# Kernel tuning notes

Hardware: AMD Instinct MI355X
Metric: run time of the kernel (lower is better)

## Reference

```python
import jax, jax.numpy as jnp
import numpy as np

EMBED_DIM = 1024
NUM_HEADS = 16
HEAD_DIM = EMBED_DIM // NUM_HEADS
EPS = 1e-6


def setup_inputs() -> dict:
    key = jax.random.key(0)
    ks = jax.random.split(key, 11)
    Lq, Lk, N = 4096, 4096, 4
    s = 1.0 / np.sqrt(EMBED_DIM)
    inp = {
        'q': jax.random.normal(ks[0], (Lq, N, EMBED_DIM), dtype=jnp.float32),
        'k': jax.random.normal(ks[1], (Lk, N, EMBED_DIM), dtype=jnp.float32),
        'v': jax.random.normal(ks[2], (Lk, N, EMBED_DIM), dtype=jnp.float32),
        'Wq': jax.random.normal(ks[3], (EMBED_DIM, EMBED_DIM), dtype=jnp.float32) * s,
        'bq': jax.random.normal(ks[4], (EMBED_DIM,), dtype=jnp.float32) * s,
        'Wk': jax.random.normal(ks[5], (EMBED_DIM, EMBED_DIM), dtype=jnp.float32) * s,
        'bk': jax.random.normal(ks[6], (EMBED_DIM,), dtype=jnp.float32) * s,
        'Wv': jax.random.normal(ks[7], (EMBED_DIM, EMBED_DIM), dtype=jnp.float32) * s,
        'bv': jax.random.normal(ks[8], (EMBED_DIM,), dtype=jnp.float32) * s,
        'Wo': jax.random.normal(ks[9], (EMBED_DIM, EMBED_DIM), dtype=jnp.float32) * s,
        'bo': jax.random.normal(ks[10], (EMBED_DIM,), dtype=jnp.float32) * s,
    }
    return inp


def _feature_map(x):
    # F.elu(x) + 1
    return jax.nn.elu(x) + 1.0


def reference(q, k, v, Wq, bq, Wk, bk, Wv, bv, Wo, bo):
    Lq, N, E = q.shape
    Lk = k.shape[0]
    # torch Linear: y = x @ W.T + b
    qp = q @ Wq.T + bq
    kp = k @ Wk.T + bk
    vp = v @ Wv.T + bv
    # (L, N, E) -> (N, H, L, D)
    qh = qp.reshape(Lq, N, NUM_HEADS, HEAD_DIM).transpose(1, 2, 0, 3)
    kh = kp.reshape(Lk, N, NUM_HEADS, HEAD_DIM).transpose(1, 2, 0, 3)
    vh = vp.reshape(Lk, N, NUM_HEADS, HEAD_DIM).transpose(1, 2, 0, 3)
    qf = _feature_map(qh)
    kf = _feature_map(kh)
    k_sum = kf.sum(axis=2)                               # (N, H, D)
    kv = jnp.einsum('nhld,nhle->nhde', kf, vh)            # (N, H, D, D)
    z = 1.0 / (jnp.einsum('nhld,nhd->nhl', qf, k_sum) + EPS)
    out = jnp.einsum('nhld,nhde->nhle', qf, kv) * z[..., None]
    out = out.transpose(2, 0, 1, 3).reshape(Lq, N, E)
    out = out @ Wo.T + bo
    return out
```

## Files before the change

kernel.cpp:

```cpp
#include <hip/hip_runtime.h>
#include <hip/hip_bf16.h>
#include <cstdint>


typedef __attribute__((ext_vector_type(8))) short bf16x8;
typedef __attribute__((ext_vector_type(4))) float f32x4;

#define L_SEQ 4096
#define NBATCH 4
#define EMB 1024
#define NHEADS 16
#define HDIM 64
#define MROWS (L_SEQ * NBATCH)
#define NHG (NBATCH * NHEADS)
#define LCHUNK 512
#define NCHUNK (L_SEQ / LCHUNK)

__device__ __forceinline__ unsigned short f2bf(float f) {
  union { float f; uint32_t u; } v; v.f = f;
  uint32_t u = v.u;
  u += 0x7fffu + ((u >> 16) & 1u);
  return (unsigned short)(u >> 16);
}
__device__ __forceinline__ float bf2f(unsigned short s) {
  union { uint32_t u; float f; } v; v.u = ((uint32_t)s) << 16;
  return v.f;
}
__device__ __forceinline__ uint32_t pkbf(float a, float b) {
  union { float f; uint32_t u; } ua, ub; ua.f = a; ub.f = b;
  return ((ua.u + 0x8000u) >> 16) | ((ub.u + 0x8000u) & 0xffff0000u);
}

__global__ __launch_bounds__(256) void convert_kernel(const float* __restrict__ src,
                                                      unsigned short* __restrict__ dst,
                                                      int n) {
  int i = (blockIdx.x * 256 + threadIdx.x) * 4;
  if (i + 4 <= n) {
    float4 f = *(const float4*)(src + i);
    uint2 p;
    p.x = pkbf(f.x, f.y);
    p.y = pkbf(f.z, f.w);
    *(uint2*)(dst + i) = p;
  }
}

__global__ __launch_bounds__(256) void convert_w4(const float* __restrict__ s0,
                                                  const float* __restrict__ s1,
                                                  const float* __restrict__ s2,
                                                  const float* __restrict__ s3,
                                                  unsigned short* __restrict__ d0,
                                                  unsigned short* __restrict__ d1,
                                                  unsigned short* __restrict__ d2,
                                                  unsigned short* __restrict__ d3,
                                                  int n) {
  const int w = blockIdx.y;
  const float* src = (w == 0) ? s0 : (w == 1) ? s1 : (w == 2) ? s2 : s3;
  unsigned short* dst = (w == 0) ? d0 : (w == 1) ? d1 : (w == 2) ? d2 : d3;
  int i = (blockIdx.x * 256 + threadIdx.x) * 4;
  if (i + 4 <= n) {
    float4 f = *(const float4*)(src + i);
    uint2 p;
    p.x = pkbf(f.x, f.y);
    p.y = pkbf(f.z, f.w);
    *(uint2*)(dst + i) = p;
  }
}


#define STAGE_H(MATB, RH, SLOT, KTN)                                            \
  do {                                                                          \
    _Pragma("unroll")                                                           \
    for (int r_ = 0; r_ < 2; r_++) {                                            \
      const long grow_ = ((MATB) ? bcol0 : arow0) + (RH) * 128 + r_ * 64 + srowt;\
      const unsigned short* gp_ =                                               \
          ((MATB) ? B : A) + grow_ * (long)K + (KTN) + skoff;                   \
      __builtin_amdgcn_global_load_lds(                                         \
          (const __attribute__((address_space(1))) void*)gp_,                   \
          (__attribute__((address_space(3))) void*)(smem + (MATB) * 65536 +     \
              (SLOT) * 16384 + r_ * 8192 + wid * 1024),                         \
          16, 0, 0);                                                            \
    }                                                                           \
  } while (0)

#define MFMA_Q(AF, BF, MFB, NFB)                                                \
  do {                                                                          \
    __builtin_amdgcn_s_setprio(1);                                              \
    _Pragma("unroll")                                                           \
    for (int mi_ = 0; mi_ < 4; mi_++)                                           \
      _Pragma("unroll")                                                         \
      for (int ni_ = 0; ni_ < 2; ni_++)                                         \
        _Pragma("unroll")                                                       \
        for (int ks_ = 0; ks_ < 2; ks_++)                                       \
          acc[(MFB) + mi_][(NFB) + ni_] =                                       \
              __builtin_amdgcn_mfma_f32_16x16x32_bf16(                          \
                  AF[mi_ * 2 + ks_], BF[ni_ * 2 + ks_],                         \
                  acc[(MFB) + mi_][(NFB) + ni_], 0, 0, 0);                      \
    __builtin_amdgcn_s_setprio(0);                                              \
  } while (0)

#define PH_SYNC                                                                 \
  __builtin_amdgcn_s_barrier();                                                 \
  asm volatile("s_waitcnt lgkmcnt(0)" ::: "memory");                            \
  __builtin_amdgcn_sched_barrier(0);

#define TILE_T(SA, K1, K2, S01, S23, VMODE)                                     \
  do {                                                                          \
    bf16x8 af0[8], af1[8], bf0[4], bf1[4];                                      \
             \
    _Pragma("unroll")                                                           \
    for (int mi_ = 0; mi_ < 4; mi_++)                                           \
      _Pragma("unroll")                                                         \
      for (int ks_ = 0; ks_ < 2; ks_++)                                         \
        af0[mi_ * 2 + ks_] = *(const bf16x8*)(smem + ((SA) + wr) * 16384 + aRB +\
                                              mi_ * 2048 + akt[ks_]);           \
    _Pragma("unroll")                                                           \
    for (int ni_ = 0; ni_ < 2; ni_++)                                           \
      _Pragma("unroll")                                                         \
      for (int ks_ = 0; ks_ < 2; ks_++)                                         \
        bf0[ni_ * 2 + ks_] = *(const bf16x8*)(smem + 65536 +                    \
                                              ((SA) + (wc >> 1)) * 16384 + bRB +\
                                              ni_ * 2048 + akt[ks_]);           \
    if (S01) STAGE_H(0, 1, (SA) ^ 3, K1);                                       \
    PH_SYNC                                                                     \
    MFMA_Q(af0, bf0, 0, 0);                                                     \
    __builtin_amdgcn_s_barrier();                                               \
                                      \
    _Pragma("unroll")                                                           \
    for (int ni_ = 0; ni_ < 2; ni_++)                                           \
      _Pragma("unroll")                                                         \
      for (int ks_ = 0; ks_ < 2; ks_++)                                         \
        bf1[ni_ * 2 + ks_] = *(const bf16x8*)(smem + 65536 +                    \
                                              ((SA) + (wc >> 1)) * 16384 + bRB +\
                                              (ni_ + 2) * 2048 + akt[ks_]);     \
    if (S01) STAGE_H(1, 1, (SA) ^ 3, K1);                                       \
    PH_SYNC                                                                     \
    MFMA_Q(af0, bf1, 0, 2);                                                     \
    __builtin_amdgcn_s_barrier();                                               \
                                  \
    _Pragma("unroll")                                                           \
    for (int mi_ = 0; mi_ < 4; mi_++)                                           \
      _Pragma("unroll")                                                         \
      for (int ks_ = 0; ks_ < 2; ks_++)                                         \
        af1[mi_ * 2 + ks_] = *(const bf16x8*)(smem + ((SA) + wr) * 16384 + aRB +\
                                              (mi_ + 4) * 2048 + akt[ks_]);     \
    if (S23) STAGE_H(1, 0, (SA), K2);                                           \
    PH_SYNC                                                                     \
    MFMA_Q(af1, bf1, 4, 2);                                                     \
    __builtin_amdgcn_s_barrier();                                               \
                     \
    if (S23) STAGE_H(0, 0, (SA), K2);                                           \
    PH_SYNC                                                                     \
    MFMA_Q(af1, bf0, 4, 0);                                                     \
    if ((VMODE) == 1) asm volatile("s_waitcnt vmcnt(4)" ::: "memory");          \
    if ((VMODE) == 2) asm volatile("s_waitcnt vmcnt(0)" ::: "memory");          \
    __builtin_amdgcn_s_barrier();                                               \
  } while (0)

template <int MODE>
__global__ __launch_bounds__(512, 2) void gemm_bt(const unsigned short* __restrict__ A,
                                                  const unsigned short* __restrict__ B,
                                                  const float* __restrict__ bias,
                                                  void* __restrict__ Cout,
                                                  int M, int Nn, int K) {
  __shared__ __align__(16) char smem[131072];

  const int tid   = threadIdx.x;
  const int wid   = tid >> 6;
  const int lane  = tid & 63;
  const int col16 = lane & 15;
  const int quad  = lane >> 4;
  const int wr = wid >> 2;
  const int wc = wid & 3;
  const long arow0 = (long)blockIdx.x * 256;
  const long bcol0 = (long)blockIdx.y * 256;

  const int axor = (col16 & 7) << 4;
  int akt[2];
  akt[0] = (quad * 16) ^ axor;
  akt[1] = (64 + quad * 16) ^ axor;
  const int aRB = col16 * 128;
  const int bRB = ((wc & 1) * 64 + col16) * 128;

  const int srowt = tid >> 3;
  const int skoff = (((tid & 7) * 16) ^ ((srowt & 7) << 4)) >> 1;

  const int NT = K >> 6;

  STAGE_H(0, 0, 0, 0);
  STAGE_H(0, 1, 1, 0);
  STAGE_H(1, 0, 0, 0);
  STAGE_H(1, 1, 1, 0);
  STAGE_H(1, 0, 2, 64);
  STAGE_H(0, 0, 2, 64);

  const f32x4 fzero = {0.f, 0.f, 0.f, 0.f};
  f32x4 acc[8][4];
#pragma unroll
  for (int i = 0; i < 8; i++)
#pragma unroll
    for (int j = 0; j < 4; j++) acc[i][j] = fzero;

  asm volatile("s_waitcnt vmcnt(4)" ::: "memory");
  __builtin_amdgcn_s_barrier();

#pragma unroll 1
  for (int u = 0; u + 4 <= NT; u += 2) {
    TILE_T(0, (u + 1) * 64, (u + 2) * 64, 1, 1, 1);
    TILE_T(2, (u + 2) * 64, (u + 3) * 64, 1, 1, 1);
  }
  TILE_T(0, (NT - 1) * 64, 0, 1, 0, 2);
  TILE_T(2, 0, 0, 0, 0, 0);

  float bcol[4];
#pragma unroll
  for (int nf = 0; nf < 4; nf++) bcol[nf] = bias[bcol0 + wc * 64 + nf * 16 + col16];

  const int erow = tid >> 4;
  const int ecc  = tid & 15;

  if (MODE != 2) {
    unsigned short* epi = (unsigned short*)smem;
    const int EST = 264;
#pragma unroll
    for (int s = 0; s < 8; s++) {
      if ((s >> 2) == wr) {
        const int mfb = (s & 3) * 2;
#pragma unroll
        for (int ml = 0; ml < 2; ml++)
#pragma unroll
          for (int nf = 0; nf < 4; nf++)
#pragma unroll
            for (int rr = 0; rr < 4; rr++) {
              float vv = acc[mfb + ml][nf][rr] + bcol[nf];
              if (MODE == 0) vv = (vv > 0.f) ? (vv + 1.f) : __expf(vv);
              epi[(ml * 16 + quad * 4 + rr) * EST + wc * 64 + nf * 16 + col16] =
                  f2bf(vv);
            }
      }
      __syncthreads();
      {
        const long gr = arow0 + s * 32 + erow;
        const unsigned short* srcp = &epi[erow * EST + ecc * 16];
        uint4 a  = *(const uint4*)srcp;
        uint4 b2 = *(const uint4*)(srcp + 8);
        unsigned short* Cp = (unsigned short*)Cout + gr * Nn + bcol0 + ecc * 16;
        *(uint4*)Cp       = a;
        *(uint4*)(Cp + 8) = b2;
      }
      __syncthreads();
    }
  } else {
    float* epi = (float*)smem;
    const int ESF = 260;
#pragma unroll
    for (int s = 0; s < 8; s++) {
      if ((s >> 2) == wr) {
        const int mfb = (s & 3) * 2;
#pragma unroll
        for (int ml = 0; ml < 2; ml++)
#pragma unroll
          for (int nf = 0; nf < 4; nf++)
#pragma unroll
            for (int rr = 0; rr < 4; rr++)
              epi[(ml * 16 + quad * 4 + rr) * ESF + wc * 64 + nf * 16 + col16] =
                  acc[mfb + ml][nf][rr] + bcol[nf];
      }
      __syncthreads();
      {
        const long gr = arow0 + s * 32 + erow;
        const float* srcp = &epi[erow * ESF + ecc * 16];
        float* Cp = (float*)Cout + gr * Nn + bcol0 + ecc * 16;
#pragma unroll
        for (int s4 = 0; s4 < 4; s4++)
          *(float4*)(Cp + s4 * 4) = *(const float4*)(srcp + s4 * 4);
      }
      __syncthreads();
    }
  }
}

__global__ __launch_bounds__(256) void kv_partial_kernel(const unsigned short* __restrict__ kf,
                                                         const unsigned short* __restrict__ vp,
                                                         float* __restrict__ kvp,
                                                         float* __restrict__ ksp) {
  __shared__ float ks[32 * 64];
  __shared__ float vs[32 * 64];
  const int hg = blockIdx.x;
  const int chunk = blockIdx.y;
  const int n = hg >> 4, h = hg & 15;
  const int tid = threadIdx.x;
  const int td = tid >> 4, te = tid & 15;
  const long hoff = (long)n * EMB + h * HDIM;
  const int l0 = chunk * LCHUNK;

  float acc[4][4];
#pragma unroll
  for (int i = 0; i < 4; i++)
#pragma unroll
    for (int j = 0; j < 4; j++) acc[i][j] = 0.f;
  float ksacc[4] = {0.f, 0.f, 0.f, 0.f};

  const int lrow = tid >> 3;
  const int dcol = (tid & 7) * 8;

  for (int ls = 0; ls < LCHUNK; ls += 32) {
    const long g = (long)(l0 + ls + lrow) * (NBATCH * EMB) + hoff + dcol;
    uint4 kr = *(const uint4*)(kf + g);
    uint4 vr = *(const uint4*)(vp + g);
    float* kd = &ks[lrow * 64 + dcol];
    float* vd = &vs[lrow * 64 + dcol];
    uint32_t ku[4] = {kr.x, kr.y, kr.z, kr.w};
    uint32_t vu[4] = {vr.x, vr.y, vr.z, vr.w};
#pragma unroll
    for (int t2 = 0; t2 < 4; t2++) {
      kd[2 * t2]     = bf2f((unsigned short)(ku[t2] & 0xffffu));
      kd[2 * t2 + 1] = bf2f((unsigned short)(ku[t2] >> 16));
      vd[2 * t2]     = bf2f((unsigned short)(vu[t2] & 0xffffu));
      vd[2 * t2 + 1] = bf2f((unsigned short)(vu[t2] >> 16));
    }
    __syncthreads();
#pragma unroll
    for (int l = 0; l < 32; l++) {
      float kq[4], vq[4];
      *(float4*)kq = *(const float4*)(&ks[l * 64 + td * 4]);
      *(float4*)vq = *(const float4*)(&vs[l * 64 + te * 4]);
#pragma unroll
      for (int i = 0; i < 4; i++) {
        ksacc[i] += kq[i];
#pragma unroll
        for (int j = 0; j < 4; j++) acc[i][j] += kq[i] * vq[j];
      }
    }
    __syncthreads();
  }
  float* outp = kvp + ((long)chunk * NHG + hg) * 4096;
#pragma unroll
  for (int i = 0; i < 4; i++)
#pragma unroll
    for (int j = 0; j < 4; j++)
      outp[(td * 4 + i) * 64 + te * 4 + j] = acc[i][j];
  if (te == 0) {
    float* o2 = ksp + ((long)chunk * NHG + hg) * 64;
#pragma unroll
    for (int i = 0; i < 4; i++) o2[td * 4 + i] = ksacc[i];
  }
}

__global__ __launch_bounds__(256) void attn_out_kernel(const unsigned short* __restrict__ qf,
                                                       const float* __restrict__ kvp,
                                                       const float* __restrict__ ksp,
                                                       unsigned short* __restrict__ out1) {
  __shared__ __align__(16) char smem[53248];
  const int hg = blockIdx.x;
  const int lc = blockIdx.y;
  const int n = hg >> 4, h = hg & 15;
  const int tid = threadIdx.x;
  const int wid = tid >> 6;
  const int lane = tid & 63;
  const int col16 = lane & 15;
  const int quad  = lane >> 4;
  const long lbase = (long)lc * 256;

#pragma unroll
  for (int r = 0; r < 8; r++) {
    const int row = r * 32 + (tid >> 3);
    const long l = lbase + row;
    const int sk = (((tid & 7) * 16) ^ ((row & 7) << 4)) >> 1;
    const unsigned short* gp = qf + (l * NBATCH + n) * (long)EMB + h * HDIM + sk;
    __builtin_amdgcn_global_load_lds(
        (const __attribute__((address_space(1))) void*)gp,
        (__attribute__((address_space(3))) void*)(smem + r * 4096 + tid * 16),
        16, 0, 0);
  }

  char* Bl = smem + 32768;
  for (int w = tid; w < 4096; w += 256) {
    const int d = w >> 6, e = w & 63;
    float s = 0.f;
#pragma unroll
    for (int c = 0; c < NCHUNK; c++) s += kvp[((long)c * NHG + hg) * 4096 + w];
    const unsigned short hi = f2bf(s);
    const unsigned short lo = f2bf(s - bf2f(hi));
    const int key = (e & 7) << 4;
    *(unsigned short*)(Bl + e * 256 + ((2 * d) ^ key))       = hi;
    *(unsigned short*)(Bl + e * 256 + ((128 + 2 * d) ^ key)) = lo;
  }
  if (tid < 64) {
    float s = 0.f;
#pragma unroll
    for (int c = 0; c < NCHUNK; c++) s += ksp[((long)c * NHG + hg) * 64 + tid];
    const unsigned short hi = f2bf(s);
    const unsigned short lo = f2bf(s - bf2f(hi));
    *(unsigned short*)(Bl + 64 * 256 + 2 * tid)       = hi;
    *(unsigned short*)(Bl + 64 * 256 + 128 + 2 * tid) = lo;
  }
  {
    uint32_t* zb = (uint32_t*)(Bl + 65 * 256);
    for (int i = tid; i < 15 * 64; i += 256) zb[i] = 0u;
  }
  __syncthreads();

  const int wl0 = wid * 64;
  const int akey = (col16 & 7) << 4;

  bf16x8 af[4][2];
#pragma unroll
  for (int mi = 0; mi < 4; mi++)
#pragma unroll
    for (int ks = 0; ks < 2; ks++)
      af[mi][ks] = *(const bf16x8*)(smem + (wl0 + mi * 16 + col16) * 128 +
                                    ((ks * 64 + quad * 16) ^ akey));

  const f32x4 fzero = {0.f, 0.f, 0.f, 0.f};
  f32x4 acc[4][5];
#pragma unroll
  for (int mi = 0; mi < 4; mi++)
#pragma unroll
    for (int nf = 0; nf < 5; nf++) acc[mi][nf] = fzero;

#pragma unroll
  for (int nf = 0; nf < 5; nf++) {
    bf16x8 bfr[4];
#pragma unroll
    for (int pass = 0; pass < 2; pass++)
#pragma unroll
      for (int ks = 0; ks < 2; ks++)
        bfr[pass * 2 + ks] = *(const bf16x8*)(Bl + (nf * 16 + col16) * 256 +
                                              ((pass * 128 + ks * 64 + quad * 16) ^ akey));
#pragma unroll
    for (int mi = 0; mi < 4; mi++)
#pragma unroll
      for (int pass = 0; pass < 2; pass++)
#pragma unroll
        for (int ks = 0; ks < 2; ks++)
          acc[mi][nf] = __builtin_amdgcn_mfma_f32_16x16x32_bf16(
              af[mi][ks], bfr[pass * 2 + ks], acc[mi][nf], 0, 0, 0);
  }

  __syncthreads();

  unsigned short* epi = (unsigned short*)smem;
#pragma unroll
  for (int mi = 0; mi < 4; mi++) {
#pragma unroll
    for (int rr = 0; rr < 4; rr++) {
      const float dv = __shfl(acc[mi][4][rr], lane & 48);
      const float z = 1.f / (dv + 1e-6f);
      const int row = wl0 + mi * 16 + quad * 4 + rr;
      const int key = (row & 7) << 4;
#pragma unroll
      for (int nf = 0; nf < 4; nf++)
        *(unsigned short*)((char*)epi + row * 128 +
                           (((nf * 16 + col16) * 2) ^ key)) =
            f2bf(acc[mi][nf][rr] * z);
    }
  }
  __syncthreads();

#pragma unroll
  for (int r = 0; r < 8; r++) {
    const int row = r * 32 + (tid >> 3);
    const long l = lbase + row;
    const uint4 vv = *(const uint4*)((char*)epi + row * 128 +
                                     (((tid & 7) * 16) ^ ((row & 7) << 4)));
    *(uint4*)(out1 + (l * NBATCH + n) * (long)EMB + h * HDIM + (tid & 7) * 8) = vv;
  }
}

extern "C" void kernel_launch(void* const* d_in, const int* in_sizes, int n_in,
                              void* d_out, int out_size, void* d_ws, size_t ws_size,
                              hipStream_t stream) {
  const float* q  = (const float*)d_in[0];
  const float* k  = (const float*)d_in[1];
  const float* v  = (const float*)d_in[2];
  const float* Wq = (const float*)d_in[3];
  const float* bq = (const float*)d_in[4];
  const float* Wk = (const float*)d_in[5];
  const float* bk = (const float*)d_in[6];
  const float* Wv = (const float*)d_in[7];
  const float* bv = (const float*)d_in[8];
  const float* Wo = (const float*)d_in[9];
  const float* bo = (const float*)d_in[10];

  char* ws = (char*)d_ws;
  const size_t BUF = (size_t)MROWS * EMB * 2;
  unsigned short* T0  = (unsigned short*)(ws);
  unsigned short* qf  = (unsigned short*)(ws + BUF);
  unsigned short* kf  = (unsigned short*)(ws + 2 * BUF);
  unsigned short* vp  = (unsigned short*)(ws + 3 * BUF);
  unsigned short* Wqb = (unsigned short*)(ws + 4 * BUF);
  unsigned short* Wkb = Wqb + (size_t)EMB * EMB;
  unsigned short* Wvb = Wkb + (size_t)EMB * EMB;
  unsigned short* Wob = Wvb + (size_t)EMB * EMB;
  float* kvp = (float*)(ws + 4 * BUF + 4 * (size_t)EMB * EMB * 2);
  float* ksp = kvp + (size_t)NCHUNK * NHG * HDIM * HDIM;

  const int nQKV = MROWS * EMB;
  const int nW   = EMB * EMB;

  convert_w4<<<dim3(nW / 1024, 4), 256, 0, stream>>>(Wq, Wk, Wv, Wo,
                                                     Wqb, Wkb, Wvb, Wob, nW);

  dim3 gg(MROWS / 256, EMB / 256), bb(512);

  convert_kernel<<<nQKV / 1024, 256, 0, stream>>>(q, T0, nQKV);
  gemm_bt<0><<<gg, bb, 0, stream>>>(T0, Wqb, bq, qf, MROWS, EMB, EMB);
  convert_kernel<<<nQKV / 1024, 256, 0, stream>>>(k, T0, nQKV);
  gemm_bt<0><<<gg, bb, 0, stream>>>(T0, Wkb, bk, kf, MROWS, EMB, EMB);
  convert_kernel<<<nQKV / 1024, 256, 0, stream>>>(v, T0, nQKV);
  gemm_bt<1><<<gg, bb, 0, stream>>>(T0, Wvb, bv, vp, MROWS, EMB, EMB);

  kv_partial_kernel<<<dim3(NHG, NCHUNK), 256, 0, stream>>>(kf, vp, kvp, ksp);
  attn_out_kernel<<<dim3(NHG, L_SEQ / 256), 256, 0, stream>>>(qf, kvp, ksp, T0);

  gemm_bt<2><<<gg, bb, 0, stream>>>(T0, Wob, bo, d_out, MROWS, EMB, EMB);
}
```

Before: 461.9 us.

## Fuse fp32-to-bf16 activation conversion into QKV projection GEMM A-tile staging

```diff
diff --git a/kernel.cpp b/kernel.cpp
--- a/kernel.cpp
+++ b/kernel.cpp
@@ -29,19 +29,6 @@
 __device__ __forceinline__ uint32_t pkbf(float a, float b) {
   union { float f; uint32_t u; } ua, ub; ua.f = a; ub.f = b;
   return ((ua.u + 0x8000u) >> 16) | ((ub.u + 0x8000u) & 0xffff0000u);
-}
-
-__global__ __launch_bounds__(256) void convert_kernel(const float* __restrict__ src,
-                                                      unsigned short* __restrict__ dst,
-                                                      int n) {
-  int i = (blockIdx.x * 256 + threadIdx.x) * 4;
-  if (i + 4 <= n) {
-    float4 f = *(const float4*)(src + i);
-    uint2 p;
-    p.x = pkbf(f.x, f.y);
-    p.y = pkbf(f.z, f.w);
-    *(uint2*)(dst + i) = p;
-  }
 }
 
 __global__ __launch_bounds__(256) void convert_w4(const float* __restrict__ s0,
@@ -82,6 +69,34 @@
     }                                                                           \
   } while (0)
 
+#define ISSUE_A32(P, RH, KTN)                                                   \
+  do {                                                                          \
+    const float* gpa_ = A32 + (arow0 + (RH) * 128 + srowt) * (long)K + (KTN) +  \
+                        (tid & 7) * 8;                                          \
+    const float* gpb_ = A32 + (arow0 + (RH) * 128 + 64 + srowt) * (long)K +     \
+                        (KTN) + (tid & 7) * 8;                                  \
+    P[0] = *(const float4*)gpa_;                                                \
+    P[1] = *(const float4*)(gpa_ + 4);                                          \
+    P[2] = *(const float4*)gpb_;                                                \
+    P[3] = *(const float4*)(gpb_ + 4);                                          \
+  } while (0)
+
+#define CVTPK(D, X, Y)                                                          \
+  asm("v_cvt_pk_bf16_f32 %0, %1, %2" : "=v"(D) : "v"(X), "v"(Y))
+
+#define WRITE_A32(P, SLOT)                                                      \
+  do {                                                                          \
+    uint32_t c0_, c1_, c2_, c3_, c4_, c5_, c6_, c7_;                            \
+    CVTPK(c0_, P[0].x, P[0].y); CVTPK(c1_, P[0].z, P[0].w);                     \
+    CVTPK(c2_, P[1].x, P[1].y); CVTPK(c3_, P[1].z, P[1].w);                     \
+    CVTPK(c4_, P[2].x, P[2].y); CVTPK(c5_, P[2].z, P[2].w);                     \
+    CVTPK(c6_, P[3].x, P[3].y); CVTPK(c7_, P[3].z, P[3].w);                     \
+    char* db_ = smem + (SLOT) * 16384 + srowt * 128 +                           \
+                (((tid & 7) * 16) ^ ((srowt & 7) << 4));                        \
+    *(uint4*)db_ = make_uint4(c0_, c1_, c2_, c3_);                              \
+    *(uint4*)(db_ + 8192) = make_uint4(c4_, c5_, c6_, c7_);                     \
+  } while (0)
+
 #define MFMA_Q(AF, BF, MFB, NFB)                                                \
   do {                                                                          \
     __builtin_amdgcn_s_setprio(1);                                              \
@@ -103,10 +118,11 @@
   asm volatile("s_waitcnt lgkmcnt(0)" ::: "memory");                            \
   __builtin_amdgcn_sched_barrier(0);
 
-#define TILE_T(SA, K1, K2, S01, S23, VMODE)                                     \
+#define TILE_T(SA, K1, K2, S01, S23, WA1, VMODE)                                \
   do {                                                                          \
     bf16x8 af0[8], af1[8], bf0[4], bf1[4];                                      \
-             \
+    float4 ah_[4];                                                              \
+                        \
     _Pragma("unroll")                                                           \
     for (int mi_ = 0; mi_ < 4; mi_++)                                           \
       _Pragma("unroll")                                                         \
@@ -120,11 +136,15 @@
         bf0[ni_ * 2 + ks_] = *(const bf16x8*)(smem + 65536 +                    \
                                               ((SA) + (wc >> 1)) * 16384 + bRB +\
                                               ni_ * 2048 + akt[ks_]);           \
-    if (S01) STAGE_H(0, 1, (SA) ^ 3, K1);                                       \
+    if constexpr (AF32) {                                                       \
+      if (S01) { ISSUE_A32(ah_, 1, K1); STAGE_H(1, 1, (SA) ^ 3, K1); }          \
+    } else {                                                                    \
+      if (S01) STAGE_H(0, 1, (SA) ^ 3, K1);                                     \
+    }                                                                           \
     PH_SYNC                                                                     \
     MFMA_Q(af0, bf0, 0, 0);                                                     \
     __builtin_amdgcn_s_barrier();                                               \
-                                      \
+                                                       \
     _Pragma("unroll")                                                           \
     for (int ni_ = 0; ni_ < 2; ni_++)                                           \
       _Pragma("unroll")                                                         \
@@ -132,7 +152,11 @@
         bf1[ni_ * 2 + ks_] = *(const bf16x8*)(smem + 65536 +                    \
                                               ((SA) + (wc >> 1)) * 16384 + bRB +\
                                               (ni_ + 2) * 2048 + akt[ks_]);     \
-    if (S01) STAGE_H(1, 1, (SA) ^ 3, K1);                                       \
+    if constexpr (AF32) {                                                       \
+      if (WA1) WRITE_A32(ap_, (SA) ^ 2);                                        \
+    } else {                                                                    \
+      if (S01) STAGE_H(1, 1, (SA) ^ 3, K1);                                     \
+    }                                                                           \
     PH_SYNC                                                                     \
     MFMA_Q(af0, bf1, 0, 2);                                                     \
     __builtin_amdgcn_s_barrier();                                               \
@@ -147,17 +171,26 @@
     PH_SYNC                                                                     \
     MFMA_Q(af1, bf1, 4, 2);                                                     \
     __builtin_amdgcn_s_barrier();                                               \
-                     \
-    if (S23) STAGE_H(0, 0, (SA), K2);                                           \
+              \
+    if constexpr (AF32) {                                                       \
+      if (S23) ISSUE_A32(ap_, 0, K2);                                           \
+      if (S01) WRITE_A32(ah_, (SA) ^ 3);                                        \
+    } else {                                                                    \
+      if (S23) STAGE_H(0, 0, (SA), K2);                                         \
+    }                                                                           \
     PH_SYNC                                                                     \
     MFMA_Q(af1, bf0, 4, 0);                                                     \
-    if ((VMODE) == 1) asm volatile("s_waitcnt vmcnt(4)" ::: "memory");          \
+    if ((VMODE) == 1) {                                                         \
+      if constexpr (AF32) asm volatile("s_waitcnt vmcnt(6)" ::: "memory");      \
+      else                asm volatile("s_waitcnt vmcnt(4)" ::: "memory");      \
+    }                                                                           \
     if ((VMODE) == 2) asm volatile("s_waitcnt vmcnt(0)" ::: "memory");          \
     __builtin_amdgcn_s_barrier();                                               \
   } while (0)
 
-template <int MODE>
+template <int MODE, int AF32>
 __global__ __launch_bounds__(512, 2) void gemm_bt(const unsigned short* __restrict__ A,
+                                                  const float* __restrict__ A32,
                                                   const unsigned short* __restrict__ B,
                                                   const float* __restrict__ bias,
                                                   void* __restrict__ Cout,
@@ -186,30 +219,50 @@
 
   const int NT = K >> 6;
 
-  STAGE_H(0, 0, 0, 0);
-  STAGE_H(0, 1, 1, 0);
-  STAGE_H(1, 0, 0, 0);
-  STAGE_H(1, 1, 1, 0);
-  STAGE_H(1, 0, 2, 64);
-  STAGE_H(0, 0, 2, 64);
+  float4 ap_[4];
 
   const f32x4 fzero = {0.f, 0.f, 0.f, 0.f};
   f32x4 acc[8][4];
-#pragma unroll
-  for (int i = 0; i < 8; i++)
-#pragma unroll
-    for (int j = 0; j < 4; j++) acc[i][j] = fzero;
-
-  asm volatile("s_waitcnt vmcnt(4)" ::: "memory");
-  __builtin_amdgcn_s_barrier();
+
+  if constexpr (AF32) {
+    {
+      float4 aw_[4];
+      ISSUE_A32(aw_, 0, 0);  WRITE_A32(aw_, 0);
+      ISSUE_A32(aw_, 1, 0);  WRITE_A32(aw_, 1);
+    }
+    STAGE_H(1, 0, 0, 0);
+    STAGE_H(1, 1, 1, 0);
+    STAGE_H(1, 0, 2, 64);
+    ISSUE_A32(ap_, 0, 64);
+#pragma unroll
+    for (int i = 0; i < 8; i++)
+#pragma unroll
+      for (int j = 0; j < 4; j++) acc[i][j] = fzero;
+    asm volatile("s_waitcnt vmcnt(6)" ::: "memory");
+    asm volatile("s_waitcnt lgkmcnt(0)" ::: "memory");
+    __builtin_amdgcn_s_barrier();
+  } else {
+    STAGE_H(0, 0, 0, 0);
+    STAGE_H(0, 1, 1, 0);
+    STAGE_H(1, 0, 0, 0);
+    STAGE_H(1, 1, 1, 0);
+    STAGE_H(1, 0, 2, 64);
+    STAGE_H(0, 0, 2, 64);
+#pragma unroll
+    for (int i = 0; i < 8; i++)
+#pragma unroll
+      for (int j = 0; j < 4; j++) acc[i][j] = fzero;
+    asm volatile("s_waitcnt vmcnt(4)" ::: "memory");
+    __builtin_amdgcn_s_barrier();
+  }
 
 #pragma unroll 1
   for (int u = 0; u + 4 <= NT; u += 2) {
-    TILE_T(0, (u + 1) * 64, (u + 2) * 64, 1, 1, 1);
-    TILE_T(2, (u + 2) * 64, (u + 3) * 64, 1, 1, 1);
-  }
-  TILE_T(0, (NT - 1) * 64, 0, 1, 0, 2);
-  TILE_T(2, 0, 0, 0, 0, 0);
+    TILE_T(0, (u + 1) * 64, (u + 2) * 64, 1, 1, 1, 1);
+    TILE_T(2, (u + 2) * 64, (u + 3) * 64, 1, 1, 1, 1);
+  }
+  TILE_T(0, (NT - 1) * 64, 0, 1, 0, 1, 2);
+  TILE_T(2, 0, 0, 0, 0, 0, 0);
 
   float bcol[4];
 #pragma unroll
@@ -495,23 +548,19 @@
   float* kvp = (float*)(ws + 4 * BUF + 4 * (size_t)EMB * EMB * 2);
   float* ksp = kvp + (size_t)NCHUNK * NHG * HDIM * HDIM;
 
-  const int nQKV = MROWS * EMB;
-  const int nW   = EMB * EMB;
+  const int nW = EMB * EMB;
 
   convert_w4<<<dim3(nW / 1024, 4), 256, 0, stream>>>(Wq, Wk, Wv, Wo,
                                                      Wqb, Wkb, Wvb, Wob, nW);
 
   dim3 gg(MROWS / 256, EMB / 256), bb(512);
 
-  convert_kernel<<<nQKV / 1024, 256, 0, stream>>>(q, T0, nQKV);
-  gemm_bt<0><<<gg, bb, 0, stream>>>(T0, Wqb, bq, qf, MROWS, EMB, EMB);
-  convert_kernel<<<nQKV / 1024, 256, 0, stream>>>(k, T0, nQKV);
-  gemm_bt<0><<<gg, bb, 0, stream>>>(T0, Wkb, bk, kf, MROWS, EMB, EMB);
-  convert_kernel<<<nQKV / 1024, 256, 0, stream>>>(v, T0, nQKV);
-  gemm_bt<1><<<gg, bb, 0, stream>>>(T0, Wvb, bv, vp, MROWS, EMB, EMB);
+  gemm_bt<0, 1><<<gg, bb, 0, stream>>>(nullptr, q, Wqb, bq, qf, MROWS, EMB, EMB);
+  gemm_bt<0, 1><<<gg, bb, 0, stream>>>(nullptr, k, Wkb, bk, kf, MROWS, EMB, EMB);
+  gemm_bt<1, 1><<<gg, bb, 0, stream>>>(nullptr, v, Wvb, bv, vp, MROWS, EMB, EMB);
 
   kv_partial_kernel<<<dim3(NHG, NCHUNK), 256, 0, stream>>>(kf, vp, kvp, ksp);
   attn_out_kernel<<<dim3(NHG, L_SEQ / 256), 256, 0, stream>>>(qf, kvp, ksp, T0);
 
-  gemm_bt<2><<<gg, bb, 0, stream>>>(T0, Wob, bo, d_out, MROWS, EMB, EMB);
-}
+  gemm_bt<2, 0><<<gg, bb, 0, stream>>>(T0, nullptr, Wob, bo, d_out, MROWS, EMB, EMB);
+}
```

Measured after the change: 573.9 us. +24.3%, slower.
